# Kernel optimization log

Measured on AMD Instinct MI355X. Metric: run time of the kernel, lower is better.

The kernel has to match this reference:

```python
import jax, jax.numpy as jnp
import numpy as np

N = 40000      # nodes
E = 320000     # edges (no self loops in input; layer adds them)
F_IN = 256
H1, C1 = 4, 128   # layer 1: att_type 'gat', concat=True
H2, C2 = 8, 6     # layer 2: att_type 'linear', concat=False (mean over heads)
BN_EPS = 1e-5
NEG_SLOPE = 0.2


def setup_inputs() -> dict:
    key = jax.random.key(0)
    k = jax.random.split(key, 12)
    x = jax.random.normal(k[0], (N, F_IN), dtype=jnp.float32)
    row = jax.random.randint(k[1], (E,), 0, N)
    off = jax.random.randint(k[2], (E,), 1, N)
    col = (row + off) % N  # guarantees no self-loops (remove_self_loops is then a no-op)
    edge_index = jnp.stack([row, col])
    s1 = 1.0 / np.sqrt(F_IN)
    s2 = 1.0 / np.sqrt(H1 * C1)
    return dict(
        x=x,
        edge_index=edge_index,
        bn1_gamma=jnp.ones((F_IN,), jnp.float32),
        bn1_beta=jnp.zeros((F_IN,), jnp.float32),
        bn1_mean=jax.random.normal(k[3], (F_IN,), jnp.float32) * 0.1,
        bn1_var=jax.random.uniform(k[4], (F_IN,), jnp.float32, 0.5, 1.5),
        W1=jax.random.normal(k[5], (F_IN, H1 * C1), jnp.float32) * s1,
        att1=jax.random.normal(k[6], (1, H1, 2 * C1), jnp.float32) * 0.1,
        b1=jnp.zeros((H1 * C1,), jnp.float32),
        bn2_gamma=jnp.ones((H1 * C1,), jnp.float32),
        bn2_beta=jnp.zeros((H1 * C1,), jnp.float32),
        bn2_mean=jax.random.normal(k[7], (H1 * C1,), jnp.float32) * 0.1,
        bn2_var=jax.random.uniform(k[8], (H1 * C1,), jnp.float32, 0.5, 1.5),
        W2=jax.random.normal(k[9], (H1 * C1, H2 * C2), jnp.float32) * s2,
        att2=jax.random.normal(k[10], (1, H2, 2 * C2), jnp.float32) * 0.1,
        b2=jnp.zeros((C2,), jnp.float32),
    )


def _bn_eval(x, gamma, beta, mean, var):
    # BatchNorm1d in eval mode (running statistics)
    return (x - mean) * (gamma / jnp.sqrt(var + BN_EPS)) + beta


def _segment_softmax(alpha, seg, num_segments):
    # stable softmax over edges grouped by destination node
    m = jax.ops.segment_max(alpha, seg, num_segments=num_segments)
    ex = jnp.exp(alpha - m[seg])
    den = jax.ops.segment_sum(ex, seg, num_segments=num_segments)
    return ex / (den[seg] + 1e-16)


def _geo_layer(x, row, col, W, att, bias, heads, out_c, att_type, concat):
    n = x.shape[0]
    h = (x @ W).reshape(n, heads, out_c)  # [N,H,C]
    h_j = h[col]                          # gather source features per edge [E,H,C]
    if att_type == 'gat':
        # (cat([x_i,x_j]) * att).sum(-1) == per-node left/right projections gathered
        a_i = (h * att[:, :, :out_c]).sum(-1)[row]   # [E,H]
        a_j = (h_j * att[:, :, out_c:]).sum(-1)      # [E,H]
        alpha = jax.nn.leaky_relu(a_i + a_j, NEG_SLOPE)
    elif att_type == 'linear':
        al = (h_j * att[:, :, :out_c]).sum(-1)
        ar = (h_j * att[:, :, out_c:]).sum(-1)
        alpha = jnp.tanh(al + ar)
    else:
        raise ValueError(att_type)
    alpha = _segment_softmax(alpha, row, n)          # neighbor softmax
    msg = h_j * alpha[:, :, None]                    # [E,H,C]
    out = jax.ops.segment_sum(msg, row, num_segments=n)  # scatter-add ('sum' agg)
    if concat:
        out = out.reshape(n, heads * out_c)
    else:
        out = out.mean(axis=1)
    return out + bias


def reference(x, edge_index, bn1_gamma, bn1_beta, bn1_mean, bn1_var, W1, att1, b1,
              bn2_gamma, bn2_beta, bn2_mean, bn2_var, W2, att2, b2):
    n = x.shape[0]
    loop = jnp.arange(n, dtype=edge_index.dtype)
    row = jnp.concatenate([edge_index[0], loop])  # add self loops (input has none)
    col = jnp.concatenate([edge_index[1], loop])
    # layer 1: dropout (identity in eval) -> BN -> GeoLayer(gat) -> act 'linear' (identity)
    out = _bn_eval(x, bn1_gamma, bn1_beta, bn1_mean, bn1_var)
    out = _geo_layer(out, row, col, W1, att1, b1, H1, C1, 'gat', True)
    # layer 2: BN -> GeoLayer(linear) -> elu
    out = _bn_eval(out, bn2_gamma, bn2_beta, bn2_mean, bn2_var)
    out = jax.nn.elu(_geo_layer(out, row, col, W2, att2, b2, H2, C2, 'linear', False))
    return jax.nn.log_softmax(out, axis=1)
```

## Files before the change

kernel.cpp:

```cpp
#include <hip/hip_runtime.h>
#include <math.h>

#define NN   40000
#define NP   40064
#define EE   320000
#define ET   (EE + NN)
#define FIN  256
#define D1   512
#define NEG  0.2f
#define CAP  64

typedef unsigned short ushort;
typedef __attribute__((ext_vector_type(8))) short   s16x8;
typedef __attribute__((ext_vector_type(4))) float   f32x4;
typedef __attribute__((ext_vector_type(4))) unsigned short u16x4;

#define GL16(g,s) __builtin_amdgcn_global_load_lds((const __attribute__((address_space(1))) unsigned*)(g), (__attribute__((address_space(3))) unsigned*)(s), 16, 0, 0)

__device__ __forceinline__ float lrelu(float x){ return x > 0.f ? x : NEG*x; }
__device__ __forceinline__ float b2f(ushort u){ return __uint_as_float(((unsigned)u) << 16); }
__device__ __forceinline__ ushort f2bf(float f){
  unsigned u = __float_as_uint(f);
  return (ushort)((u + 0x7fffu + ((u >> 16) & 1u)) >> 16);
}
__device__ __forceinline__ float wmaxf(float v){
#pragma unroll
  for (int o = 32; o > 0; o >>= 1) v = fmaxf(v, __shfl_xor(v, o));
  return v;
}
__device__ __forceinline__ float wsumf(float v){
#pragma unroll
  for (int o = 32; o > 0; o >>= 1) v += __shfl_xor(v, o);
  return v;
}

__global__ __launch_bounds__(1024) void zero_prep_kernel(int* __restrict__ cnt,
                            const float* __restrict__ g1, const float* __restrict__ be1,
                            const float* __restrict__ mu1, const float* __restrict__ va1,
                            const float* __restrict__ g2, const float* __restrict__ be2,
                            const float* __restrict__ mu2, const float* __restrict__ va2,
                            const float* __restrict__ b1,
                            float* __restrict__ sc1, float* __restrict__ sh1,
                            float* __restrict__ sc2, float* __restrict__ sh2)
{
  int i = blockIdx.x*1024 + threadIdx.x;
  if (i < NN) cnt[i] = 0;
  if (blockIdx.x == 0){
    int t = threadIdx.x;
    if (t < FIN){ float s = g1[t]*rsqrtf(va1[t]+1e-5f); sc1[t]=s; sh1[t]=be1[t]-mu1[t]*s; }
    if (t < D1){ float s = g2[t]*rsqrtf(va2[t]+1e-5f); sc2[t]=s; sh2[t]=be2[t]+(b1[t]-mu2[t])*s; }
  }
}

__global__ __launch_bounds__(256) void prep_all_kernel(
    const int* __restrict__ rows, const int* __restrict__ cols,
    int* __restrict__ cnt, int* __restrict__ cs,
    const float* __restrict__ W1, const float* __restrict__ W2,
    const float* __restrict__ sc1, const float* __restrict__ sh1,
    const float* __restrict__ sc2, const float* __restrict__ sh2,
    const float* __restrict__ att1, const float* __restrict__ att2,
    ushort* __restrict__ K1T, float* __restrict__ k0v,
    float* __restrict__ c2, float* __restrict__ a2s)
{
  int b = blockIdx.x;
  if (b < 1407){
    int e = b*256 + threadIdx.x;
    if (e >= ET) return;
    int r, c;
    if (e < EE){ r = rows[e]; c = cols[e]; } else { r = e - EE; c = r; }
    int slot = atomicAdd(&cnt[r], 1);
    if (slot < CAP) cs[(r << 6) + slot] = c;
    return;
  }
  if (b < 1631){
    __shared__ float wcol[128];
    __shared__ float red[4];
    int t = b - 1407;
    int k = threadIdx.x;
    float val = 0.f;
    if (t < 200){
      int h;
      if (t < 192){
        h = t & 3; int j = t >> 2;
        if (k < 128){ int kk = h*128 + k; wcol[k] = W2[(size_t)kk*48 + j] * sc2[kk]; }
      } else {
        h = (t - 192) & 3; int off = ((t - 192) >= 4) ? 128 : 0;
        if (k < 128) wcol[k] = att1[h*256 + off + k];
      }
      __syncthreads();
      const float* wr = W1 + (size_t)k*D1 + h*128;
#pragma unroll
      for (int kk = 0; kk < 128; kk += 4){
        float4 wv = *(const float4*)(wr + kk);
        float4 cv = *(const float4*)(wcol + kk);
        val += wv.x*cv.x + wv.y*cv.y + wv.z*cv.z + wv.w*cv.w;
      }
      K1T[(size_t)t*FIN + k] = f2bf(val * sc1[k]);
      float part = wsumf(sh1[k] * val);
      if ((k & 63) == 0) red[k >> 6] = part;
      __syncthreads();
      if (k == 0) k0v[t] = red[0] + red[1] + red[2] + red[3];
    } else {
      K1T[(size_t)t*FIN + k] = 0;
      if (k == 0) k0v[t] = 0.f;
    }
    return;
  }
  {
    int bb = b - 1631;
    if (bb == 0 && threadIdx.x < 48){
      int h = threadIdx.x/6, c = threadIdx.x%6;
      a2s[threadIdx.x] = att2[h*12 + c] + att2[h*12 + 6 + c];
    }
    int w = bb*4 + (threadIdx.x >> 6);
    int lane = threadIdx.x & 63;
    if (w >= 48) return;
    float acc = 0.f;
    for (int k = lane; k < D1; k += 64) acc += sh2[k] * W2[(size_t)k*48 + w];
    acc = wsumf(acc);
    if (lane == 0) c2[w] = acc;
  }
}

__global__ __launch_bounds__(256) void gemmG_mfma(const float* __restrict__ X,
                                                  const ushort* __restrict__ K1T,
                                                  const float* __restrict__ k0v,
                                                  ushort* __restrict__ G,
                                                  float* __restrict__ ai,
                                                  float* __restrict__ aj)
{
  __shared__ ushort As[64*64];
  __shared__ ushort Bs[224*64];
  int row0 = blockIdx.x * 64;
  int tid = threadIdx.x, lane = tid & 63, wave = tid >> 6;
  f32x4 acc[13] = {};
  int srow = lane >> 3;
  int scolb = (lane & 7) * 16;
#pragma unroll
  for (int kt = 0; kt < 4; ++kt){
    int k0 = kt*64;
#pragma unroll
    for (int j = 0; j < 2; ++j){
      int c = wave*2 + j;
      int rl = c*8 + srow;
      int rowg = row0 + rl; if (rowg >= NN) rowg = 0;
      int j0 = ((lane & 7) ^ (rl & 7)) * 8;
      const float* src = X + (size_t)rowg*FIN + k0 + j0;
      float4 v0 = *(const float4*)src;
      float4 v1 = *(const float4*)(src + 4);
      s16x8 o;
      o[0]=(short)f2bf(v0.x); o[1]=(short)f2bf(v0.y); o[2]=(short)f2bf(v0.z); o[3]=(short)f2bf(v0.w);
      o[4]=(short)f2bf(v1.x); o[5]=(short)f2bf(v1.y); o[6]=(short)f2bf(v1.z); o[7]=(short)f2bf(v1.w);
      *(s16x8*)((char*)As + c*1024 + lane*16) = o;
    }
#pragma unroll
    for (int j = 0; j < 7; ++j){
      int c = wave*7 + j;
      int row = c*8 + srow;
      int cb = scolb ^ ((row & 7) << 4);
      GL16((const char*)(K1T + (size_t)row*FIN + k0) + cb, (char*)Bs + c*1024);
    }
    __syncthreads();
#pragma unroll
    for (int kk = 0; kk < 2; ++kk){
      int kb = kk*64 + (lane >> 4)*16;
      int arow = wave*16 + (lane & 15);
      s16x8 a = *(const s16x8*)((const char*)As + arow*128 + (kb ^ ((arow & 7) << 4)));
#pragma unroll
      for (int ni = 0; ni < 13; ++ni){
        int row = ni*16 + (lane & 15);
        s16x8 bfrag = *(const s16x8*)((const char*)Bs + row*128 + (kb ^ ((row & 7) << 4)));
        acc[ni] = __builtin_amdgcn_mfma_f32_16x16x32_bf16(a, bfrag, acc[ni], 0, 0, 0);
      }
    }
    __syncthreads();
  }
  int cl = lane & 15;
#pragma unroll
  for (int ni = 0; ni < 12; ++ni){
    int t = ni*16 + cl;
    float kc = k0v[t];
#pragma unroll
    for (int rr = 0; rr < 4; ++rr){
      int row = row0 + wave*16 + (lane >> 4)*4 + rr;
      G[(size_t)row*192 + t] = f2bf(acc[ni][rr] + kc);
    }
  }
  if (cl < 8){
    float kc = k0v[192 + cl];
#pragma unroll
    for (int rr = 0; rr < 4; ++rr){
      int row = row0 + wave*16 + (lane >> 4)*4 + rr;
      float v = acc[12][rr] + kc;
      if (cl < 4) ai[(size_t)row*4 + cl] = v;
      else        aj[(size_t)row*4 + (cl-4)] = v;
    }
  }
}

__global__ __launch_bounds__(256) void aggA_kernel(const ushort* __restrict__ G,
                                                   const float* __restrict__ ai,
                                                   const float* __restrict__ aj,
                                                   const int* __restrict__ cnt,
                                                   const int* __restrict__ cs,
                                                   const float* __restrict__ c2,
                                                   const float* __restrict__ a2s,
                                                   ushort* __restrict__ PE)
{
  __shared__ float wsh[4][64][4];
  __shared__ int   csh[4][64];
  int lane = threadIdx.x & 63;
  int wave = threadIdx.x >> 6;
  int n = blockIdx.x*4 + wave;
  int deg = cnt[n]; deg = deg > CAP ? CAP : deg;
  float4 an = *(const float4*)(ai + (size_t)n*4);
  bool aclane = lane < 48;
  int lidx = aclane ? lane : 0;
  const char* Gb = (const char*)G + (size_t)lidx*8;
  float acc = 0.f;

  bool act = lane < deg;
  int c = 0;
  float sx=-1e30f, sy=-1e30f, sz=-1e30f, sw=-1e30f;
  if (act){
    c = cs[(n << 6) + lane];
    float4 av = *(const float4*)(aj + (size_t)c*4);
    sx = lrelu(an.x+av.x); sy = lrelu(an.y+av.y);
    sz = lrelu(an.z+av.z); sw = lrelu(an.w+av.w);
  }
  float m0 = wmaxf(sx), m1 = wmaxf(sy), m2 = wmaxf(sz), m3 = wmaxf(sw);
  float e0 = act ? __expf(sx-m0) : 0.f;
  float e1 = act ? __expf(sy-m1) : 0.f;
  float e2 = act ? __expf(sz-m2) : 0.f;
  float e3 = act ? __expf(sw-m3) : 0.f;
  float d0 = wsumf(e0)+1e-16f, d1 = wsumf(e1)+1e-16f;
  float d2 = wsumf(e2)+1e-16f, d3 = wsumf(e3)+1e-16f;
  if (act){
    wsh[wave][lane][0] = e0/d0; wsh[wave][lane][1] = e1/d1;
    wsh[wave][lane][2] = e2/d2; wsh[wave][lane][3] = e3/d3;
    csh[wave][lane] = c*384;
  }
  int e = 0;
  for (; e + 8 <= deg; e += 8){
    int   ob[8];
    u16x4 vb[8];
#pragma unroll
    for (int q = 0; q < 8; ++q) ob[q] = csh[wave][e+q];
#pragma unroll
    for (int q = 0; q < 8; ++q) vb[q] = *(const u16x4*)(Gb + ob[q]);
#pragma unroll
    for (int q = 0; q < 8; ++q){
      float4 w = *(const float4*)wsh[wave][e+q];
      u16x4 v = vb[q];
      acc += w.x*b2f(v[0]) + w.y*b2f(v[1]) + w.z*b2f(v[2]) + w.w*b2f(v[3]);
    }
  }
  for (; e + 4 <= deg; e += 4){
    int o0 = csh[wave][e],   o1_ = csh[wave][e+1];
    int o2 = csh[wave][e+2], o3  = csh[wave][e+3];
    float4 w0 = *(const float4*)wsh[wave][e];
    float4 w1 = *(const float4*)wsh[wave][e+1];
    float4 w2 = *(const float4*)wsh[wave][e+2];
    float4 w3 = *(const float4*)wsh[wave][e+3];
    u16x4 v0 = *(const u16x4*)(Gb + o0);
    u16x4 v1 = *(const u16x4*)(Gb + o1_);
    u16x4 v2 = *(const u16x4*)(Gb + o2);
    u16x4 v3 = *(const u16x4*)(Gb + o3);
    acc += w0.x*b2f(v0[0]) + w0.y*b2f(v0[1]) + w0.z*b2f(v0[2]) + w0.w*b2f(v0[3]);
    acc += w1.x*b2f(v1[0]) + w1.y*b2f(v1[1]) + w1.z*b2f(v1[2]) + w1.w*b2f(v1[3]);
    acc += w2.x*b2f(v2[0]) + w2.y*b2f(v2[1]) + w2.z*b2f(v2[2]) + w2.w*b2f(v2[3]);
    acc += w3.x*b2f(v3[0]) + w3.y*b2f(v3[1]) + w3.z*b2f(v3[2]) + w3.w*b2f(v3[3]);
  }
  for (; e < deg; ++e){
    int o0 = csh[wave][e];
    float4 w0 = *(const float4*)wsh[wave][e];
    u16x4 v0 = *(const u16x4*)(Gb + o0);
    acc += w0.x*b2f(v0[0]) + w0.y*b2f(v0[1]) + w0.z*b2f(v0[2]) + w0.w*b2f(v0[3]);
  }

  float h = acc + (aclane ? c2[lidx] : 0.f);
  float s = h * (aclane ? a2s[lidx] : 0.f);
  float tot = 0.f;
  int base = (lane/6)*6;
#pragma unroll
  for (int i = 0; i < 6; ++i) tot += __shfl(s, base + i);
  if (aclane){
    float eh = __expf(tanhf(tot));
    ushort* pe = PE + ((size_t)n << 6);
    pe[lane] = f2bf(eh * h);
    if ((lane % 6) == 0) pe[48 + lane/6] = f2bf(eh);
  }
}

__global__ __launch_bounds__(256) void agg2_kernel(const ushort* __restrict__ PE,
                                                   const int* __restrict__ cnt,
                                                   const int* __restrict__ cs,
                                                   const float* __restrict__ bias2,
                                                   float* __restrict__ out)
{
  __shared__ int csh[4][64];
  int lane = threadIdx.x & 63;
  int wave = threadIdx.x >> 6;
  int n = blockIdx.x*4 + wave;
  int deg = cnt[n]; deg = deg > CAP ? CAP : deg;
  int lidx = (lane < 56) ? lane : 0;
  const char* PEb = (const char*)PE + (size_t)lidx*2;
  float acc = 0.f;

  if (lane < deg) csh[wave][lane] = cs[(n << 6) + lane] << 7;
  int e = 0;
  for (; e + 8 <= deg; e += 8){
    int ob[8]; ushort vb[8];
#pragma unroll
    for (int q = 0; q < 8; ++q) ob[q] = csh[wave][e+q];
#pragma unroll
    for (int q = 0; q < 8; ++q) vb[q] = *(const ushort*)(PEb + ob[q]);
#pragma unroll
    for (int q = 0; q < 8; ++q) acc += b2f(vb[q]);
  }
  for (; e + 4 <= deg; e += 4){
    int o0 = csh[wave][e],   o1_ = csh[wave][e+1];
    int o2 = csh[wave][e+2], o3  = csh[wave][e+3];
    float v0 = b2f(*(const ushort*)(PEb + o0));
    float v1 = b2f(*(const ushort*)(PEb + o1_));
    float v2 = b2f(*(const ushort*)(PEb + o2));
    float v3 = b2f(*(const ushort*)(PEb + o3));
    acc += (v0 + v1) + (v2 + v3);
  }
  for (; e < deg; ++e)
    acc += b2f(*(const ushort*)(PEb + csh[wave][e]));

  int hh = (lane < 48) ? lane/6 : 0;
  float den = __shfl(acc, 48 + hh);
  float v = acc / den;
  int cc = lane % 6;
  float s = 0.f;
#pragma unroll
  for (int qq = 0; qq < 8; ++qq) s += __shfl(v, cc + 6*qq);
  float val0 = s*(1.f/8.f) + bias2[cc];
  val0 = val0 > 0.f ? val0 : (__expf(val0) - 1.f);
  float val = (lane < 6) ? val0 : -1e30f;
  float mx = val;
#pragma unroll
  for (int o = 1; o < 8; o <<= 1) mx = fmaxf(mx, __shfl_xor(mx, o));
  float ex = (lane < 6) ? __expf(val - mx) : 0.f;
#pragma unroll
  for (int o = 1; o < 8; o <<= 1) ex += __shfl_xor(ex, o);
  if (lane < 6) out[(size_t)n*6 + lane] = val - mx - __logf(ex);
}

extern "C" void kernel_launch(void* const* d_in, const int* in_sizes, int n_in,
                              void* d_out, int out_size, void* d_ws, size_t ws_size,
                              hipStream_t stream)
{
  (void)in_sizes; (void)n_in; (void)out_size; (void)ws_size;
  const float* x   = (const float*)d_in[0];
  const int*   ei  = (const int*)  d_in[1];
  const float* g1  = (const float*)d_in[2];
  const float* be1 = (const float*)d_in[3];
  const float* mu1 = (const float*)d_in[4];
  const float* va1 = (const float*)d_in[5];
  const float* W1  = (const float*)d_in[6];
  const float* at1 = (const float*)d_in[7];
  const float* b1  = (const float*)d_in[8];
  const float* g2  = (const float*)d_in[9];
  const float* be2 = (const float*)d_in[10];
  const float* mu2 = (const float*)d_in[11];
  const float* va2 = (const float*)d_in[12];
  const float* W2  = (const float*)d_in[13];
  const float* at2 = (const float*)d_in[14];
  const float* b2  = (const float*)d_in[15];
  const int* rows = ei;
  const int* cols = ei + EE;
  float* out = (float*)d_out;

  char* p = (char*)d_ws;
  auto carve = [&](size_t bytes)->void*{ void* r = (void*)p; p += (bytes + 255) & ~(size_t)255; return r; };
  ushort* K1T = (ushort*)carve((size_t)224*FIN*2);
  ushort* G   = (ushort*)carve((size_t)NP*192*2);
  ushort* PE  = (ushort*)carve((size_t)NN*64*2);
  float* k0v  = (float*)carve(224*4);
  float* c2   = (float*)carve(48*4);
  float* a2s  = (float*)carve(48*4);
  float* ai   = (float*)carve((size_t)NP*4*4);
  float* aj   = (float*)carve((size_t)NP*4*4);
  float* sc1  = (float*)carve(FIN*4);
  float* sh1  = (float*)carve(FIN*4);
  float* sc2  = (float*)carve(D1*4);
  float* sh2  = (float*)carve(D1*4);
  int* cnt    = (int*)carve((size_t)NN*4);
  int* cs     = (int*)carve((size_t)NN*CAP*4);

  zero_prep_kernel<<<40, 1024, 0, stream>>>(cnt, g1,be1,mu1,va1,g2,be2,mu2,va2,b1,
                                            sc1,sh1,sc2,sh2);
  prep_all_kernel<<<1643, 256, 0, stream>>>(rows, cols, cnt, cs,
                                            W1, W2, sc1, sh1, sc2, sh2, at1, at2,
                                            K1T, k0v, c2, a2s);
  gemmG_mfma<<<626, 256, 0, stream>>>(x, K1T, k0v, G, ai, aj);
  aggA_kernel<<<NN/4, 256, 0, stream>>>(G, ai, aj, cnt, cs, c2, a2s, PE);
  agg2_kernel<<<NN/4, 256, 0, stream>>>(PE, cnt, cs, b2, out);
}
```

Measured before the change: 101.6 us.

## Process two nodes per wave in aggregation kernels with branchless padded gathers

```diff
diff --git a/kernel.cpp b/kernel.cpp
--- a/kernel.cpp
+++ b/kernel.cpp
@@ -23,11 +23,6 @@
   unsigned u = __float_as_uint(f);
   return (ushort)((u + 0x7fffu + ((u >> 16) & 1u)) >> 16);
 }
-__device__ __forceinline__ float wmaxf(float v){
-#pragma unroll
-  for (int o = 32; o > 0; o >>= 1) v = fmaxf(v, __shfl_xor(v, o));
-  return v;
-}
 __device__ __forceinline__ float wsumf(float v){
 #pragma unroll
   for (int o = 32; o > 0; o >>= 1) v += __shfl_xor(v, o);
@@ -35,6 +30,7 @@
 }
 
 __global__ __launch_bounds__(1024) void zero_prep_kernel(int* __restrict__ cnt,
+                            ushort* __restrict__ PE,
                             const float* __restrict__ g1, const float* __restrict__ be1,
                             const float* __restrict__ mu1, const float* __restrict__ va1,
                             const float* __restrict__ g2, const float* __restrict__ be2,
@@ -49,6 +45,7 @@
     int t = threadIdx.x;
     if (t < FIN){ float s = g1[t]*rsqrtf(va1[t]+1e-5f); sc1[t]=s; sh1[t]=be1[t]-mu1[t]*s; }
     if (t < D1){ float s = g2[t]*rsqrtf(va2[t]+1e-5f); sc2[t]=s; sh2[t]=be2[t]+(b1[t]-mu2[t])*s; }
+    if (t < 64) PE[((size_t)NN << 6) + t] = 0;
   }
 }
 
@@ -207,88 +204,86 @@
                                                    const float* __restrict__ a2s,
                                                    ushort* __restrict__ PE)
 {
-  __shared__ float wsh[4][64][4];
-  __shared__ int   csh[4][64];
+  __shared__ float wsh[4][2][64][4];
+  __shared__ int   csh[4][2][64];
   int lane = threadIdx.x & 63;
   int wave = threadIdx.x >> 6;
-  int n = blockIdx.x*4 + wave;
-  int deg = cnt[n]; deg = deg > CAP ? CAP : deg;
-  float4 an = *(const float4*)(ai + (size_t)n*4);
+  int n0 = blockIdx.x*8 + wave*2;
+  int n1 = n0 + 1;
+  int deg0 = cnt[n0]; deg0 = deg0 > CAP ? CAP : deg0;
+  int deg1 = cnt[n1]; deg1 = deg1 > CAP ? CAP : deg1;
+  float4 an0 = *(const float4*)(ai + (size_t)n0*4);
+  float4 an1 = *(const float4*)(ai + (size_t)n1*4);
   bool aclane = lane < 48;
   int lidx = aclane ? lane : 0;
   const char* Gb = (const char*)G + (size_t)lidx*8;
-  float acc = 0.f;
-
-  bool act = lane < deg;
-  int c = 0;
-  float sx=-1e30f, sy=-1e30f, sz=-1e30f, sw=-1e30f;
-  if (act){
-    c = cs[(n << 6) + lane];
-    float4 av = *(const float4*)(aj + (size_t)c*4);
-    sx = lrelu(an.x+av.x); sy = lrelu(an.y+av.y);
-    sz = lrelu(an.z+av.z); sw = lrelu(an.w+av.w);
-  }
-  float m0 = wmaxf(sx), m1 = wmaxf(sy), m2 = wmaxf(sz), m3 = wmaxf(sw);
-  float e0 = act ? __expf(sx-m0) : 0.f;
-  float e1 = act ? __expf(sy-m1) : 0.f;
-  float e2 = act ? __expf(sz-m2) : 0.f;
-  float e3 = act ? __expf(sw-m3) : 0.f;
-  float d0 = wsumf(e0)+1e-16f, d1 = wsumf(e1)+1e-16f;
-  float d2 = wsumf(e2)+1e-16f, d3 = wsumf(e3)+1e-16f;
-  if (act){
-    wsh[wave][lane][0] = e0/d0; wsh[wave][lane][1] = e1/d1;
-    wsh[wave][lane][2] = e2/d2; wsh[wave][lane][3] = e3/d3;
-    csh[wave][lane] = c*384;
-  }
-  int e = 0;
-  for (; e + 8 <= deg; e += 8){
-    int   ob[8];
-    u16x4 vb[8];
-#pragma unroll
-    for (int q = 0; q < 8; ++q) ob[q] = csh[wave][e+q];
-#pragma unroll
-    for (int q = 0; q < 8; ++q) vb[q] = *(const u16x4*)(Gb + ob[q]);
-#pragma unroll
-    for (int q = 0; q < 8; ++q){
-      float4 w = *(const float4*)wsh[wave][e+q];
-      u16x4 v = vb[q];
-      acc += w.x*b2f(v[0]) + w.y*b2f(v[1]) + w.z*b2f(v[2]) + w.w*b2f(v[3]);
-    }
-  }
-  for (; e + 4 <= deg; e += 4){
-    int o0 = csh[wave][e],   o1_ = csh[wave][e+1];
-    int o2 = csh[wave][e+2], o3  = csh[wave][e+3];
-    float4 w0 = *(const float4*)wsh[wave][e];
-    float4 w1 = *(const float4*)wsh[wave][e+1];
-    float4 w2 = *(const float4*)wsh[wave][e+2];
-    float4 w3 = *(const float4*)wsh[wave][e+3];
-    u16x4 v0 = *(const u16x4*)(Gb + o0);
-    u16x4 v1 = *(const u16x4*)(Gb + o1_);
-    u16x4 v2 = *(const u16x4*)(Gb + o2);
-    u16x4 v3 = *(const u16x4*)(Gb + o3);
-    acc += w0.x*b2f(v0[0]) + w0.y*b2f(v0[1]) + w0.z*b2f(v0[2]) + w0.w*b2f(v0[3]);
-    acc += w1.x*b2f(v1[0]) + w1.y*b2f(v1[1]) + w1.z*b2f(v1[2]) + w1.w*b2f(v1[3]);
-    acc += w2.x*b2f(v2[0]) + w2.y*b2f(v2[1]) + w2.z*b2f(v2[2]) + w2.w*b2f(v2[3]);
-    acc += w3.x*b2f(v3[0]) + w3.y*b2f(v3[1]) + w3.z*b2f(v3[2]) + w3.w*b2f(v3[3]);
-  }
-  for (; e < deg; ++e){
-    int o0 = csh[wave][e];
-    float4 w0 = *(const float4*)wsh[wave][e];
-    u16x4 v0 = *(const u16x4*)(Gb + o0);
-    acc += w0.x*b2f(v0[0]) + w0.y*b2f(v0[1]) + w0.z*b2f(v0[2]) + w0.w*b2f(v0[3]);
-  }
-
-  float h = acc + (aclane ? c2[lidx] : 0.f);
-  float s = h * (aclane ? a2s[lidx] : 0.f);
-  float tot = 0.f;
+
+  bool a0 = lane < deg0, a1 = lane < deg1;
+  int c0 = 0, c1 = 0;
+  float e00=0,e01=0,e02=0,e03=0, e10=0,e11=0,e12=0,e13=0;
+  if (a0){
+    c0 = cs[(n0 << 6) + lane];
+    float4 av = *(const float4*)(aj + (size_t)c0*4);
+    e00 = __expf(lrelu(an0.x+av.x)); e01 = __expf(lrelu(an0.y+av.y));
+    e02 = __expf(lrelu(an0.z+av.z)); e03 = __expf(lrelu(an0.w+av.w));
+  }
+  if (a1){
+    c1 = cs[(n1 << 6) + lane];
+    float4 av = *(const float4*)(aj + (size_t)c1*4);
+    e10 = __expf(lrelu(an1.x+av.x)); e11 = __expf(lrelu(an1.y+av.y));
+    e12 = __expf(lrelu(an1.z+av.z)); e13 = __expf(lrelu(an1.w+av.w));
+  }
+  float d00 = wsumf(e00)+1e-16f, d01 = wsumf(e01)+1e-16f;
+  float d02 = wsumf(e02)+1e-16f, d03 = wsumf(e03)+1e-16f;
+  float d10 = wsumf(e10)+1e-16f, d11 = wsumf(e11)+1e-16f;
+  float d12 = wsumf(e12)+1e-16f, d13 = wsumf(e13)+1e-16f;
+  wsh[wave][0][lane][0]=e00; wsh[wave][0][lane][1]=e01;
+  wsh[wave][0][lane][2]=e02; wsh[wave][0][lane][3]=e03;
+  wsh[wave][1][lane][0]=e10; wsh[wave][1][lane][1]=e11;
+  wsh[wave][1][lane][2]=e12; wsh[wave][1][lane][3]=e13;
+  csh[wave][0][lane] = a0 ? c0*384 : 0;
+  csh[wave][1][lane] = a1 ? c1*384 : 0;
+
+  float A00=0,A01=0,A02=0,A03=0, A10=0,A11=0,A12=0,A13=0;
+  int dm = deg0 > deg1 ? deg0 : deg1;
+  for (int e = 0; e < dm; e += 2){
+    int o00 = csh[wave][0][e], o01 = csh[wave][0][e+1];
+    int o10 = csh[wave][1][e], o11 = csh[wave][1][e+1];
+    u16x4 v00 = *(const u16x4*)(Gb + o00);
+    u16x4 v01 = *(const u16x4*)(Gb + o01);
+    u16x4 v10 = *(const u16x4*)(Gb + o10);
+    u16x4 v11 = *(const u16x4*)(Gb + o11);
+    float4 w00 = *(const float4*)wsh[wave][0][e];
+    float4 w01 = *(const float4*)wsh[wave][0][e+1];
+    float4 w10 = *(const float4*)wsh[wave][1][e];
+    float4 w11 = *(const float4*)wsh[wave][1][e+1];
+    A00 += w00.x*b2f(v00[0]) + w01.x*b2f(v01[0]);
+    A01 += w00.y*b2f(v00[1]) + w01.y*b2f(v01[1]);
+    A02 += w00.z*b2f(v00[2]) + w01.z*b2f(v01[2]);
+    A03 += w00.w*b2f(v00[3]) + w01.w*b2f(v01[3]);
+    A10 += w10.x*b2f(v10[0]) + w11.x*b2f(v11[0]);
+    A11 += w10.y*b2f(v10[1]) + w11.y*b2f(v11[1]);
+    A12 += w10.z*b2f(v10[2]) + w11.z*b2f(v11[2]);
+    A13 += w10.w*b2f(v10[3]) + w11.w*b2f(v11[3]);
+  }
+
+  float cc2 = aclane ? c2[lidx] : 0.f;
+  float aa2 = aclane ? a2s[lidx] : 0.f;
+  float h0 = A00/d00 + A01/d01 + A02/d02 + A03/d03 + cc2;
+  float h1_ = A10/d10 + A11/d11 + A12/d12 + A13/d13 + cc2;
+  float s0 = h0*aa2, s1 = h1_*aa2;
+  float t0 = 0.f, t1 = 0.f;
   int base = (lane/6)*6;
 #pragma unroll
-  for (int i = 0; i < 6; ++i) tot += __shfl(s, base + i);
+  for (int i = 0; i < 6; ++i){ t0 += __shfl(s0, base + i); t1 += __shfl(s1, base + i); }
   if (aclane){
-    float eh = __expf(tanhf(tot));
-    ushort* pe = PE + ((size_t)n << 6);
-    pe[lane] = f2bf(eh * h);
-    if ((lane % 6) == 0) pe[48 + lane/6] = f2bf(eh);
+    float eh0 = __expf(tanhf(t0));
+    float eh1 = __expf(tanhf(t1));
+    ushort* pe0 = PE + ((size_t)n0 << 6);
+    ushort* pe1 = PE + ((size_t)n1 << 6);
+    pe0[lane] = f2bf(eh0*h0);
+    pe1[lane] = f2bf(eh1*h1_);
+    if ((lane % 6) == 0){ pe0[48 + lane/6] = f2bf(eh0); pe1[48 + lane/6] = f2bf(eh1); }
   }
 }
 
@@ -298,55 +293,57 @@
                                                    const float* __restrict__ bias2,
                                                    float* __restrict__ out)
 {
-  __shared__ int csh[4][64];
+  __shared__ int csh[4][2][64];
   int lane = threadIdx.x & 63;
   int wave = threadIdx.x >> 6;
-  int n = blockIdx.x*4 + wave;
-  int deg = cnt[n]; deg = deg > CAP ? CAP : deg;
+  int n0 = blockIdx.x*8 + wave*2;
+  int n1 = n0 + 1;
+  int deg0 = cnt[n0]; deg0 = deg0 > CAP ? CAP : deg0;
+  int deg1 = cnt[n1]; deg1 = deg1 > CAP ? CAP : deg1;
   int lidx = (lane < 56) ? lane : 0;
   const char* PEb = (const char*)PE + (size_t)lidx*2;
-  float acc = 0.f;
-
-  if (lane < deg) csh[wave][lane] = cs[(n << 6) + lane] << 7;
-  int e = 0;
-  for (; e + 8 <= deg; e += 8){
-    int ob[8]; ushort vb[8];
-#pragma unroll
-    for (int q = 0; q < 8; ++q) ob[q] = csh[wave][e+q];
-#pragma unroll
-    for (int q = 0; q < 8; ++q) vb[q] = *(const ushort*)(PEb + ob[q]);
-#pragma unroll
-    for (int q = 0; q < 8; ++q) acc += b2f(vb[q]);
-  }
-  for (; e + 4 <= deg; e += 4){
-    int o0 = csh[wave][e],   o1_ = csh[wave][e+1];
-    int o2 = csh[wave][e+2], o3  = csh[wave][e+3];
-    float v0 = b2f(*(const ushort*)(PEb + o0));
-    float v1 = b2f(*(const ushort*)(PEb + o1_));
-    float v2 = b2f(*(const ushort*)(PEb + o2));
-    float v3 = b2f(*(const ushort*)(PEb + o3));
-    acc += (v0 + v1) + (v2 + v3);
-  }
-  for (; e < deg; ++e)
-    acc += b2f(*(const ushort*)(PEb + csh[wave][e]));
+  const int ZOFF = NN << 7;
+  csh[wave][0][lane] = (lane < deg0) ? (cs[(n0 << 6) + lane] << 7) : ZOFF;
+  csh[wave][1][lane] = (lane < deg1) ? (cs[(n1 << 6) + lane] << 7) : ZOFF;
+  float acc0 = 0.f, acc1 = 0.f;
+  int dm = deg0 > deg1 ? deg0 : deg1;
+  for (int e = 0; e < dm; e += 2){
+    int o00 = csh[wave][0][e], o01 = csh[wave][0][e+1];
+    int o10 = csh[wave][1][e], o11 = csh[wave][1][e+1];
+    float v00 = b2f(*(const ushort*)(PEb + o00));
+    float v01 = b2f(*(const ushort*)(PEb + o01));
+    float v10 = b2f(*(const ushort*)(PEb + o10));
+    float v11 = b2f(*(const ushort*)(PEb + o11));
+    acc0 += v00 + v01;
+    acc1 += v10 + v11;
+  }
 
   int hh = (lane < 48) ? lane/6 : 0;
-  float den = __shfl(acc, 48 + hh);
-  float v = acc / den;
+  float den0 = __shfl(acc0, 48 + hh);
+  float den1 = __shfl(acc1, 48 + hh);
+  float v0 = acc0 / den0, v1 = acc1 / den1;
   int cc = lane % 6;
-  float s = 0.f;
-#pragma unroll
-  for (int qq = 0; qq < 8; ++qq) s += __shfl(v, cc + 6*qq);
-  float val0 = s*(1.f/8.f) + bias2[cc];
-  val0 = val0 > 0.f ? val0 : (__expf(val0) - 1.f);
-  float val = (lane < 6) ? val0 : -1e30f;
-  float mx = val;
-#pragma unroll
-  for (int o = 1; o < 8; o <<= 1) mx = fmaxf(mx, __shfl_xor(mx, o));
-  float ex = (lane < 6) ? __expf(val - mx) : 0.f;
-#pragma unroll
-  for (int o = 1; o < 8; o <<= 1) ex += __shfl_xor(ex, o);
-  if (lane < 6) out[(size_t)n*6 + lane] = val - mx - __logf(ex);
+  float s0 = 0.f, s1 = 0.f;
+#pragma unroll
+  for (int qq = 0; qq < 8; ++qq){ s0 += __shfl(v0, cc + 6*qq); s1 += __shfl(v1, cc + 6*qq); }
+  float bb = bias2[cc];
+  float u0 = s0*(1.f/8.f) + bb;
+  float u1 = s1*(1.f/8.f) + bb;
+  u0 = u0 > 0.f ? u0 : (__expf(u0) - 1.f);
+  u1 = u1 > 0.f ? u1 : (__expf(u1) - 1.f);
+  float val0 = (lane < 6) ? u0 : -1e30f;
+  float val1 = (lane < 6) ? u1 : -1e30f;
+  float mx0 = val0, mx1 = val1;
+#pragma unroll
+  for (int o = 1; o < 8; o <<= 1){ mx0 = fmaxf(mx0, __shfl_xor(mx0, o)); mx1 = fmaxf(mx1, __shfl_xor(mx1, o)); }
+  float ex0 = (lane < 6) ? __expf(val0 - mx0) : 0.f;
+  float ex1 = (lane < 6) ? __expf(val1 - mx1) : 0.f;
+#pragma unroll
+  for (int o = 1; o < 8; o <<= 1){ ex0 += __shfl_xor(ex0, o); ex1 += __shfl_xor(ex1, o); }
+  if (lane < 6){
+    out[(size_t)n0*6 + lane] = val0 - mx0 - __logf(ex0);
+    out[(size_t)n1*6 + lane] = val1 - mx1 - __logf(ex1);
+  }
 }
 
 extern "C" void kernel_launch(void* const* d_in, const int* in_sizes, int n_in,
@@ -378,7 +375,7 @@
   auto carve = [&](size_t bytes)->void*{ void* r = (void*)p; p += (bytes + 255) & ~(size_t)255; return r; };
   ushort* K1T = (ushort*)carve((size_t)224*FIN*2);
   ushort* G   = (ushort*)carve((size_t)NP*192*2);
-  ushort* PE  = (ushort*)carve((size_t)NN*64*2);
+  ushort* PE  = (ushort*)carve((size_t)(NN+1)*64*2);
   float* k0v  = (float*)carve(224*4);
   float* c2   = (float*)carve(48*4);
   float* a2s  = (float*)carve(48*4);
@@ -391,12 +388,12 @@
   int* cnt    = (int*)carve((size_t)NN*4);
   int* cs     = (int*)carve((size_t)NN*CAP*4);
 
-  zero_prep_kernel<<<40, 1024, 0, stream>>>(cnt, g1,be1,mu1,va1,g2,be2,mu2,va2,b1,
+  zero_prep_kernel<<<40, 1024, 0, stream>>>(cnt, PE, g1,be1,mu1,va1,g2,be2,mu2,va2,b1,
                                             sc1,sh1,sc2,sh2);
   prep_all_kernel<<<1643, 256, 0, stream>>>(rows, cols, cnt, cs,
                                             W1, W2, sc1, sh1, sc2, sh2, at1, at2,
                                             K1T, k0v, c2, a2s);
   gemmG_mfma<<<626, 256, 0, stream>>>(x, K1T, k0v, G, ai, aj);
-  aggA_kernel<<<NN/4, 256, 0, stream>>>(G, ai, aj, cnt, cs, c2, a2s, PE);
-  agg2_kernel<<<NN/4, 256, 0, stream>>>(PE, cnt, cs, b2, out);
-}
+  aggA_kernel<<<NN/8, 256, 0, stream>>>(G, ai, aj, cnt, cs, c2, a2s, PE);
+  agg2_kernel<<<NN/8, 256, 0, stream>>>(PE, cnt, cs, b2, out);
+}
```

Measured after the change: 97.71 us (median of 2 runs). 3.9% less time.
